# Performance work log

Hardware: AMD Instinct MI355X
Metric: run time of the kernel (lower is better)

The kernel has to match this reference:

```python
import jax, jax.numpy as jnp
import numpy as np

N, C, LM, ELEMS = 1024, 128, 16, 10   # nodes, channels, lm components (lmax=3), elements
P1, P2, P3 = 4, 12, 30                # generalized-CG path counts per correlation order
DIMS = (1, 3)                         # output irreps kept: 0e (dim 1), 1o (dim 3)


def _sparse(rng, shape, density=0.15):
    # stand-in generalized Clebsch-Gordan U tensor: fixed, sparse constants
    a = rng.standard_normal(shape).astype(np.float32)
    return jnp.asarray(a * (rng.random(shape) < density))


def setup_inputs() -> dict:
    k = jax.random.split(jax.random.key(0), 2)
    rng = np.random.default_rng(0)
    inp = {
        'x': jax.random.normal(k[0], (N, C, LM), jnp.float32),
        'species': jax.random.randint(k[1], (N,), 0, ELEMS, jnp.int32),
    }
    for i, d in enumerate(DIMS):
        inp[f'U1_{i}'] = _sparse(rng, (d, LM, P1))
        inp[f'U2_{i}'] = _sparse(rng, (d, LM, LM, P2))
        inp[f'U3_{i}'] = _sparse(rng, (d, LM, LM, LM, P3))
        for nu, p in ((1, P1), (2, P2), (3, P3)):
            inp[f'W{nu}_{i}'] = jnp.asarray((rng.standard_normal((ELEMS, p, C)) / np.sqrt(p)).astype(np.float32))
        inp[f'Wlin_{i}'] = jnp.asarray(rng.standard_normal((C, C)).astype(np.float32))
    return inp


def _sym_contract(x, species, U1, U2, U3, W1, W2, W3):
    # MACE recursive symmetric contraction, highest correlation order first.
    # x: [n, c, m] (channels factored to separate axis); species selects per-element weights.
    out = jnp.einsum('Lijmp,npc,ncm->ncLij', U3, W3[species], x)          # nu = 3 term
    out = jnp.einsum('Lijp,npc->ncLij', U2, W2[species]) + out            # add nu = 2 basis
    out = jnp.einsum('ncLij,ncj->ncLi', out, x)                           # contract one power of x
    out = jnp.einsum('Lip,npc->ncLi', U1, W1[species]) + out              # add nu = 1 basis
    return jnp.einsum('ncLi,nci->ncL', out, x)                            # [n, c, dim_L]


def _forward(x, species, U1_0, U2_0, U3_0, W1_0, W2_0, W3_0, Wlin_0,
             U1_1, U2_1, U3_1, W1_1, W2_1, W3_1, Wlin_1):
    f0 = _sym_contract(x, species, U1_0, U2_0, U3_0, W1_0, W2_0, W3_0)    # [n, C, 1]
    f1 = _sym_contract(x, species, U1_1, U2_1, U3_1, W1_1, W2_1, W3_1)    # [n, C, 3]
    s = 1.0 / float(np.sqrt(C))                                            # e3nn.Linear path norm
    y0 = jnp.einsum('nc,ck->nk', f0[..., 0], Wlin_0) * s                  # 128x0e block
    y1 = jnp.einsum('nci,ck->nki', f1, Wlin_1) * s                        # 128x1o block
    return jnp.concatenate([y0, y1.reshape(y1.shape[0], -1)], axis=-1)    # [n, 128 + 384]


def reference(x, species, U1_0, U2_0, U3_0, W1_0, W2_0, W3_0, Wlin_0,
              U1_1, U2_1, U3_1, W1_1, W2_1, W3_1, Wlin_1):
    return _forward(x, species, U1_0, U2_0, U3_0, W1_0, W2_0, W3_0, Wlin_0,
                    U1_1, U2_1, U3_1, W1_1, W2_1, W3_1, Wlin_1)
```

## Files before the change

### kernel.cpp

```cpp
#include <hip/hip_runtime.h>

typedef float v2f __attribute__((ext_vector_type(2)));

#define NN    1024
#define CC    128
#define NELEM 10
#define NQ3   816
#define NQ2   136
#define NQ    968
#define KP    48
#define QT    22

#define NL_OFF    0
#define CNT_OFF   40960
#define CALL_OFF  524288
#define F_OFF     20447232
#define UHAT_OFF  20447232

__device__ __constant__ int d_OFF2[16] = {0,16,31,45,58,70,81,91,100,108,115,121,126,130,133,135};
__device__ __constant__ int d_OFF3[16] = {0,136,256,361,452,530,596,651,696,732,760,781,796,806,812,815};

__global__ void k_usym3(const float* __restrict__ U3_0, const float* __restrict__ U3_1,
                        float* __restrict__ uhat) {
    int tid = blockIdx.x * 256 + threadIdx.x;
    if (tid >= 4 * 4096) return;
    int Lout = tid >> 12;
    int r = tid & 4095;
    int a = r >> 8, b = (r >> 4) & 15, m = r & 15;
    if (a > b || b > m) return;
    int q = d_OFF3[a] + (d_OFF2[b] - d_OFF2[a]) + (m - b);
    const float* U = (Lout == 0) ? U3_0 : U3_1;
    int L = (Lout == 0) ? 0 : (Lout - 1);
    int P[6][3] = {{a,b,m},{a,m,b},{b,a,m},{b,m,a},{m,a,b},{m,b,a}};
    float s[30];
#pragma unroll
    for (int p = 0; p < 30; ++p) s[p] = 0.f;
    for (int t = 0; t < 6; ++t) {
        bool dup = false;
        for (int u = 0; u < t; ++u)
            if (P[u][0] == P[t][0] && P[u][1] == P[t][1] && P[u][2] == P[t][2]) dup = true;
        if (dup) continue;
        const float* src = U + ((((L * 16 + P[t][0]) * 16 + P[t][1]) * 16 + P[t][2]) * 30);
#pragma unroll
        for (int p = 0; p < 30; ++p) s[p] += src[p];
    }
    float* dst = uhat + ((size_t)Lout * NQ + q) * KP;
#pragma unroll
    for (int p = 0; p < 30; ++p) dst[p] = s[p];
#pragma unroll
    for (int p = 30; p < KP; ++p) dst[p] = 0.f;
}

__global__ void k_usym2lin(const float* __restrict__ U2_0, const float* __restrict__ U2_1,
                           const float* __restrict__ U1_0, const float* __restrict__ U1_1,
                           float* __restrict__ uhat) {
    int tid = blockIdx.x * 256 + threadIdx.x;
    if (tid < 1024) {
        int Lout = tid >> 8;
        int r = tid & 255;
        int a = r >> 4, b = r & 15;
        if (a > b) return;
        int q = NQ3 + d_OFF2[a] + (b - a);
        const float* U = (Lout == 0) ? U2_0 : U2_1;
        int L = (Lout == 0) ? 0 : (Lout - 1);
        float* dst = uhat + ((size_t)Lout * NQ + q) * KP;
#pragma unroll
        for (int p = 0; p < 30; ++p) dst[p] = 0.f;
#pragma unroll
        for (int p = 0; p < 12; ++p) {
            float v = U[((L * 16 + a) * 16 + b) * 12 + p];
            if (a != b) v += U[((L * 16 + b) * 16 + a) * 12 + p];
            dst[30 + p] = v;
        }
#pragma unroll
        for (int p = 42; p < KP; ++p) dst[p] = 0.f;
    } else if (tid < 1024 + 64) {
        int s2 = tid - 1024;
        int Lout = s2 >> 4, i = s2 & 15;
        int q = NQ3 + NQ2 + i;
        const float* U = (Lout == 0) ? U1_0 : U1_1;
        int L = (Lout == 0) ? 0 : (Lout - 1);
        float* dst = uhat + ((size_t)Lout * NQ + q) * KP;
#pragma unroll
        for (int p = 0; p < 42; ++p) dst[p] = 0.f;
#pragma unroll
        for (int p = 0; p < 4; ++p) dst[42 + p] = U[(L * 16 + i) * 4 + p];
        dst[46] = 0.f; dst[47] = 0.f;
    }
}

__global__ void k_plist(const int* __restrict__ species, int* __restrict__ nodelist,
                        int* __restrict__ counts) {
    __shared__ int cnt[NELEM];
    int t = threadIdx.x;
    if (t < NELEM) cnt[t] = 0;
    __syncthreads();
    int e = species[t];
    int pos = atomicAdd(&cnt[e], 1);
    nodelist[e * NN + pos] = t;
    __syncthreads();
    if (t < NELEM) counts[t] = cnt[t];
}

__global__ __launch_bounds__(256) void k_fold(
    const float* __restrict__ uhat,
    const float* __restrict__ W1_0, const float* __restrict__ W2_0, const float* __restrict__ W3_0,
    const float* __restrict__ W1_1, const float* __restrict__ W2_1, const float* __restrict__ W3_1,
    float4* __restrict__ call4) {
    __shared__ __align__(16) float uh_lds[4][QT][KP];
    int e  = blockIdx.x / 44;
    int qt = blockIdx.x % 44;
    int t = threadIdx.x;
    {
        const float4* src4 = (const float4*)uhat;
        float4* dst4 = (float4*)uh_lds;
        for (int i = t; i < 4 * QT * 12; i += 256) {
            int l = i / (QT * 12);
            int r = i - l * (QT * 12);
            int qloc = r / 12, p4 = r % 12;
            dst4[i] = src4[((size_t)l * NQ + qt * QT + qloc) * 12 + p4];
        }
    }
    int c  = t & 127;
    int qs = t >> 7;
    float wr[2][KP];
#pragma unroll
    for (int p = 0; p < 30; ++p) {
        wr[0][p] = W3_0[(e * 30 + p) * CC + c];
        wr[1][p] = W3_1[(e * 30 + p) * CC + c];
    }
#pragma unroll
    for (int p = 0; p < 12; ++p) {
        wr[0][30 + p] = W2_0[(e * 12 + p) * CC + c];
        wr[1][30 + p] = W2_1[(e * 12 + p) * CC + c];
    }
#pragma unroll
    for (int p = 0; p < 4; ++p) {
        wr[0][42 + p] = W1_0[(e * 4 + p) * CC + c];
        wr[1][42 + p] = W1_1[(e * 4 + p) * CC + c];
    }
    wr[0][46] = wr[0][47] = wr[1][46] = wr[1][47] = 0.f;
    __syncthreads();
    size_t base = ((size_t)e * CC + c) * NQ;
    for (int j = 0; j < 11; ++j) {
        int qloc = qs * 11 + j;
        int q = qt * QT + qloc;
        float r[4];
#pragma unroll
        for (int l = 0; l < 4; ++l) {
            const float4* up = (const float4*)uh_lds[l][qloc];
            const float* w = (l == 0) ? wr[0] : wr[1];
            float acc0 = 0.f, acc1 = 0.f, acc2 = 0.f, acc3 = 0.f;
#pragma unroll
            for (int p4 = 0; p4 < 12; ++p4) {
                float4 u = up[p4];
                acc0 = fmaf(u.x, w[p4 * 4 + 0], acc0);
                acc1 = fmaf(u.y, w[p4 * 4 + 1], acc1);
                acc2 = fmaf(u.z, w[p4 * 4 + 2], acc2);
                acc3 = fmaf(u.w, w[p4 * 4 + 3], acc3);
            }
            r[l] = (acc0 + acc1) + (acc2 + acc3);
        }
        call4[base + q] = make_float4(r[0], r[1], r[2], r[3]);
    }
}

#define CUBIC(A0, A1) { \
    _Pragma("unroll") for (int a = (A0); a < (A1); ++a) { \
        _Pragma("unroll") for (int b = a; b < 16; ++b) { \
            v2f pab = xv[a] * xv[b]; \
            _Pragma("unroll") for (int m = b; m < 16; ++m) { \
                float4 w = cf_lds[q]; v2f mo = pab * xv[m]; \
                a0 += mo * w.x; a1 += mo * w.y; a2 += mo * w.z; a3 += mo * w.w; ++q; } } } }

#define QUAD(A0, A1) { \
    _Pragma("unroll") for (int a = (A0); a < (A1); ++a) { \
        _Pragma("unroll") for (int b = a; b < 16; ++b) { \
            float4 w = cf_lds[q]; v2f mo = xv[a] * xv[b]; \
            a0 += mo * w.x; a1 += mo * w.y; a2 += mo * w.z; a3 += mo * w.w; ++q; } } }

__global__ __launch_bounds__(256, 4) void k_eval(
    const float* __restrict__ x, const int* __restrict__ nodelist,
    const int* __restrict__ counts, const float4* __restrict__ call4,
    float4* __restrict__ fout) {
    __shared__ __align__(16) float4 cf_lds[NQ];
    __shared__ __align__(16) v2f part[3][64][4];
    int ec = blockIdx.x;
    int e = ec >> 7;
    int c = ec & 127;
    int cnt = counts[e];
    const float4* cf = call4 + (size_t)ec * NQ;
    int t = threadIdx.x;
    for (int i = t; i < NQ; i += 256) cf_lds[i] = cf[i];
    __syncthreads();
    int slice = t >> 6;
    int lane  = t & 63;

    for (int sb = 0; sb < cnt; sb += 128) {
        int i0 = sb + lane * 2, i1 = i0 + 1;
        bool v0i = i0 < cnt, v1i = i1 < cnt;
        int n0 = v0i ? nodelist[e * NN + i0] : 0;
        int n1 = v1i ? nodelist[e * NN + i1] : 0;
        const float4* xp0 = (const float4*)(x + ((size_t)n0 * CC + c) * 16);
        const float4* xp1 = (const float4*)(x + ((size_t)n1 * CC + c) * 16);
        float4 p0 = xp0[0], p1 = xp0[1], p2 = xp0[2], p3 = xp0[3];
        float4 q0 = xp1[0], q1 = xp1[1], q2 = xp1[2], q3 = xp1[3];
        v2f xv[16];
        xv[0]  = v2f{p0.x, q0.x}; xv[1]  = v2f{p0.y, q0.y};
        xv[2]  = v2f{p0.z, q0.z}; xv[3]  = v2f{p0.w, q0.w};
        xv[4]  = v2f{p1.x, q1.x}; xv[5]  = v2f{p1.y, q1.y};
        xv[6]  = v2f{p1.z, q1.z}; xv[7]  = v2f{p1.w, q1.w};
        xv[8]  = v2f{p2.x, q2.x}; xv[9]  = v2f{p2.y, q2.y};
        xv[10] = v2f{p2.z, q2.z}; xv[11] = v2f{p2.w, q2.w};
        xv[12] = v2f{p3.x, q3.x}; xv[13] = v2f{p3.y, q3.y};
        xv[14] = v2f{p3.z, q3.z}; xv[15] = v2f{p3.w, q3.w};
        if (!v0i) {
#pragma unroll
            for (int m = 0; m < 16; ++m) xv[m].x = 0.f;
        }
        if (!v1i) {
#pragma unroll
            for (int m = 0; m < 16; ++m) xv[m].y = 0.f;
        }
        v2f a0 = {0.f, 0.f}, a1 = {0.f, 0.f}, a2 = {0.f, 0.f}, a3 = {0.f, 0.f};
        int q;
        if (slice == 0) {
            q = 0;   CUBIC(0, 2);
        } else if (slice == 1) {
            q = 256; CUBIC(2, 4);
            q = NQ3; QUAD(0, 4);
        } else if (slice == 2) {
            q = 452; CUBIC(4, 7);
            q = NQ3 + 58; QUAD(4, 10);
        } else {
            q = 651; CUBIC(7, 16);
            q = NQ3 + 115; QUAD(10, 16);
            q = NQ3 + NQ2;
#pragma unroll
            for (int a = 0; a < 16; ++a) {
                float4 w = cf_lds[q]; v2f mo = xv[a];
                a0 += mo * w.x; a1 += mo * w.y; a2 += mo * w.z; a3 += mo * w.w; ++q;
            }
        }
        if (slice > 0) {
            part[slice - 1][lane][0] = a0; part[slice - 1][lane][1] = a1;
            part[slice - 1][lane][2] = a2; part[slice - 1][lane][3] = a3;
        }
        __syncthreads();
        if (slice == 0) {
            v2f s0 = a0 + part[0][lane][0] + part[1][lane][0] + part[2][lane][0];
            v2f s1 = a1 + part[0][lane][1] + part[1][lane][1] + part[2][lane][1];
            v2f s2 = a2 + part[0][lane][2] + part[1][lane][2] + part[2][lane][2];
            v2f s3 = a3 + part[0][lane][3] + part[1][lane][3] + part[2][lane][3];
            if (v0i) fout[(size_t)n0 * CC + c] = make_float4(s0.x, s1.x, s2.x, s3.x);
            if (v1i) fout[(size_t)n1 * CC + c] = make_float4(s0.y, s1.y, s2.y, s3.y);
        }
        __syncthreads();
    }
}

__global__ __launch_bounds__(256) void k_linear(
    const float4* __restrict__ fin, const float* __restrict__ Wlin0,
    const float* __restrict__ Wlin1, float* __restrict__ out) {
    __shared__ float4 fl[256];
    int t = threadIdx.x;
    fl[t] = fin[(size_t)blockIdx.x * 256 + t];
    __syncthreads();
    int nl = t >> 7, k = t & 127;
    int n = blockIdx.x * 2 + nl;
    float a0 = 0.f, a1 = 0.f, a2 = 0.f, a3 = 0.f;
#pragma unroll 8
    for (int c = 0; c < CC; ++c) {
        float4 f = fl[nl * CC + c];
        float w0 = Wlin0[c * CC + k];
        float w1 = Wlin1[c * CC + k];
        a0 = fmaf(f.x, w0, a0);
        a1 = fmaf(f.y, w1, a1);
        a2 = fmaf(f.z, w1, a2);
        a3 = fmaf(f.w, w1, a3);
    }
    const float s = 0.08838834764831845f;
    float* o = out + (size_t)n * 512;
    o[k] = a0 * s;
    o[128 + 3 * k + 0] = a1 * s;
    o[128 + 3 * k + 1] = a2 * s;
    o[128 + 3 * k + 2] = a3 * s;
}

extern "C" void kernel_launch(void* const* d_in, const int* in_sizes, int n_in,
                              void* d_out, int out_size, void* d_ws, size_t ws_size,
                              hipStream_t stream) {
    const float* x     = (const float*)d_in[0];
    const int*   spec  = (const int*)d_in[1];
    const float* U1_0  = (const float*)d_in[2];
    const float* U2_0  = (const float*)d_in[3];
    const float* U3_0  = (const float*)d_in[4];
    const float* W1_0  = (const float*)d_in[5];
    const float* W2_0  = (const float*)d_in[6];
    const float* W3_0  = (const float*)d_in[7];
    const float* Wl_0  = (const float*)d_in[8];
    const float* U1_1  = (const float*)d_in[9];
    const float* U2_1  = (const float*)d_in[10];
    const float* U3_1  = (const float*)d_in[11];
    const float* W1_1  = (const float*)d_in[12];
    const float* W2_1  = (const float*)d_in[13];
    const float* W3_1  = (const float*)d_in[14];
    const float* Wl_1  = (const float*)d_in[15];

    char* ws = (char*)d_ws;
    int*    nodelist = (int*)(ws + NL_OFF);
    int*    counts   = (int*)(ws + CNT_OFF);
    float4* call4    = (float4*)(ws + CALL_OFF);
    float*  uhat     = (float*)(ws + UHAT_OFF);
    float4* fbuf     = (float4*)(ws + F_OFF);

    k_usym3<<<dim3(64), dim3(256), 0, stream>>>(U3_0, U3_1, uhat);
    k_usym2lin<<<dim3(5), dim3(256), 0, stream>>>(U2_0, U2_1, U1_0, U1_1, uhat);
    k_plist<<<dim3(1), dim3(1024), 0, stream>>>(spec, nodelist, counts);
    k_fold<<<dim3(440), dim3(256), 0, stream>>>(uhat, W1_0, W2_0, W3_0,
                                                W1_1, W2_1, W3_1, call4);
    k_eval<<<dim3(1280), dim3(256), 0, stream>>>(x, nodelist, counts, call4, fbuf);
    k_linear<<<dim3(512), dim3(256), 0, stream>>>(fbuf, Wl_0, Wl_1, (float*)d_out);
}
```

Before: 88.39 us.

## Store folded coefficients in fp16, merge U kernels, retile fold, prefetch eval inputs

The per-(element,channel) folded coefficient table is now written and read as packed half2 pairs, halving its global and LDS footprint. The two U-symmetrization kernels are merged into one launch, the fold kernel uses smaller q tiles to double its block count, and the eval kernel issues its node-list and x loads before waiting on the coefficient LDS fill. The fp16 rounding of coefficients lowers accuracy and may break the tolerance. Removing the min-occupancy launch bound may also change register allocation.

```diff
diff --git a/kernel.cpp b/kernel.cpp
--- a/kernel.cpp
+++ b/kernel.cpp
@@ -1,4 +1,5 @@
 #include <hip/hip_runtime.h>
+#include <hip/hip_fp16.h>
 
 typedef float v2f __attribute__((ext_vector_type(2)));
 
@@ -9,83 +10,83 @@
 #define NQ2   136
 #define NQ    968
 #define KP    48
-#define QT    22
+#define QT    11
+#define NTILE 88
 
 #define NL_OFF    0
 #define CNT_OFF   40960
 #define CALL_OFF  524288
 #define F_OFF     20447232
-#define UHAT_OFF  20447232
+#define UHAT_OFF  10485760
 
 __device__ __constant__ int d_OFF2[16] = {0,16,31,45,58,70,81,91,100,108,115,121,126,130,133,135};
 __device__ __constant__ int d_OFF3[16] = {0,136,256,361,452,530,596,651,696,732,760,781,796,806,812,815};
 
-__global__ void k_usym3(const float* __restrict__ U3_0, const float* __restrict__ U3_1,
-                        float* __restrict__ uhat) {
-    int tid = blockIdx.x * 256 + threadIdx.x;
-    if (tid >= 4 * 4096) return;
-    int Lout = tid >> 12;
-    int r = tid & 4095;
-    int a = r >> 8, b = (r >> 4) & 15, m = r & 15;
-    if (a > b || b > m) return;
-    int q = d_OFF3[a] + (d_OFF2[b] - d_OFF2[a]) + (m - b);
-    const float* U = (Lout == 0) ? U3_0 : U3_1;
-    int L = (Lout == 0) ? 0 : (Lout - 1);
-    int P[6][3] = {{a,b,m},{a,m,b},{b,a,m},{b,m,a},{m,a,b},{m,b,a}};
-    float s[30];
-#pragma unroll
-    for (int p = 0; p < 30; ++p) s[p] = 0.f;
-    for (int t = 0; t < 6; ++t) {
-        bool dup = false;
-        for (int u = 0; u < t; ++u)
-            if (P[u][0] == P[t][0] && P[u][1] == P[t][1] && P[u][2] == P[t][2]) dup = true;
-        if (dup) continue;
-        const float* src = U + ((((L * 16 + P[t][0]) * 16 + P[t][1]) * 16 + P[t][2]) * 30);
-#pragma unroll
-        for (int p = 0; p < 30; ++p) s[p] += src[p];
-    }
-    float* dst = uhat + ((size_t)Lout * NQ + q) * KP;
-#pragma unroll
-    for (int p = 0; p < 30; ++p) dst[p] = s[p];
-#pragma unroll
-    for (int p = 30; p < KP; ++p) dst[p] = 0.f;
-}
-
-__global__ void k_usym2lin(const float* __restrict__ U2_0, const float* __restrict__ U2_1,
-                           const float* __restrict__ U1_0, const float* __restrict__ U1_1,
-                           float* __restrict__ uhat) {
-    int tid = blockIdx.x * 256 + threadIdx.x;
-    if (tid < 1024) {
-        int Lout = tid >> 8;
-        int r = tid & 255;
-        int a = r >> 4, b = r & 15;
-        if (a > b) return;
-        int q = NQ3 + d_OFF2[a] + (b - a);
-        const float* U = (Lout == 0) ? U2_0 : U2_1;
+__global__ void k_usym(const float* __restrict__ U3_0, const float* __restrict__ U3_1,
+                       const float* __restrict__ U2_0, const float* __restrict__ U2_1,
+                       const float* __restrict__ U1_0, const float* __restrict__ U1_1,
+                       float* __restrict__ uhat) {
+    if (blockIdx.x < 64) {
+        int tid = blockIdx.x * 256 + threadIdx.x;
+        int Lout = tid >> 12;
+        int r = tid & 4095;
+        int a = r >> 8, b = (r >> 4) & 15, m = r & 15;
+        if (a > b || b > m) return;
+        int q = d_OFF3[a] + (d_OFF2[b] - d_OFF2[a]) + (m - b);
+        const float* U = (Lout == 0) ? U3_0 : U3_1;
         int L = (Lout == 0) ? 0 : (Lout - 1);
+        int P[6][3] = {{a,b,m},{a,m,b},{b,a,m},{b,m,a},{m,a,b},{m,b,a}};
+        float s[30];
+#pragma unroll
+        for (int p = 0; p < 30; ++p) s[p] = 0.f;
+        for (int t = 0; t < 6; ++t) {
+            bool dup = false;
+            for (int u = 0; u < t; ++u)
+                if (P[u][0] == P[t][0] && P[u][1] == P[t][1] && P[u][2] == P[t][2]) dup = true;
+            if (dup) continue;
+            const float* src = U + ((((L * 16 + P[t][0]) * 16 + P[t][1]) * 16 + P[t][2]) * 30);
+#pragma unroll
+            for (int p = 0; p < 30; ++p) s[p] += src[p];
+        }
         float* dst = uhat + ((size_t)Lout * NQ + q) * KP;
 #pragma unroll
-        for (int p = 0; p < 30; ++p) dst[p] = 0.f;
-#pragma unroll
-        for (int p = 0; p < 12; ++p) {
-            float v = U[((L * 16 + a) * 16 + b) * 12 + p];
-            if (a != b) v += U[((L * 16 + b) * 16 + a) * 12 + p];
-            dst[30 + p] = v;
-        }
-#pragma unroll
-        for (int p = 42; p < KP; ++p) dst[p] = 0.f;
-    } else if (tid < 1024 + 64) {
-        int s2 = tid - 1024;
-        int Lout = s2 >> 4, i = s2 & 15;
-        int q = NQ3 + NQ2 + i;
-        const float* U = (Lout == 0) ? U1_0 : U1_1;
-        int L = (Lout == 0) ? 0 : (Lout - 1);
-        float* dst = uhat + ((size_t)Lout * NQ + q) * KP;
-#pragma unroll
-        for (int p = 0; p < 42; ++p) dst[p] = 0.f;
-#pragma unroll
-        for (int p = 0; p < 4; ++p) dst[42 + p] = U[(L * 16 + i) * 4 + p];
-        dst[46] = 0.f; dst[47] = 0.f;
+        for (int p = 0; p < 30; ++p) dst[p] = s[p];
+#pragma unroll
+        for (int p = 30; p < KP; ++p) dst[p] = 0.f;
+    } else {
+        int tid = (blockIdx.x - 64) * 256 + threadIdx.x;
+        if (tid < 1024) {
+            int Lout = tid >> 8;
+            int r = tid & 255;
+            int a = r >> 4, b = r & 15;
+            if (a > b) return;
+            int q = NQ3 + d_OFF2[a] + (b - a);
+            const float* U = (Lout == 0) ? U2_0 : U2_1;
+            int L = (Lout == 0) ? 0 : (Lout - 1);
+            float* dst = uhat + ((size_t)Lout * NQ + q) * KP;
+#pragma unroll
+            for (int p = 0; p < 30; ++p) dst[p] = 0.f;
+#pragma unroll
+            for (int p = 0; p < 12; ++p) {
+                float v = U[((L * 16 + a) * 16 + b) * 12 + p];
+                if (a != b) v += U[((L * 16 + b) * 16 + a) * 12 + p];
+                dst[30 + p] = v;
+            }
+#pragma unroll
+            for (int p = 42; p < KP; ++p) dst[p] = 0.f;
+        } else if (tid < 1024 + 64) {
+            int s2 = tid - 1024;
+            int Lout = s2 >> 4, i = s2 & 15;
+            int q = NQ3 + NQ2 + i;
+            const float* U = (Lout == 0) ? U1_0 : U1_1;
+            int L = (Lout == 0) ? 0 : (Lout - 1);
+            float* dst = uhat + ((size_t)Lout * NQ + q) * KP;
+#pragma unroll
+            for (int p = 0; p < 42; ++p) dst[p] = 0.f;
+#pragma unroll
+            for (int p = 0; p < 4; ++p) dst[42 + p] = U[(L * 16 + i) * 4 + p];
+            dst[46] = 0.f; dst[47] = 0.f;
+        }
     }
 }
 
@@ -106,10 +107,10 @@
     const float* __restrict__ uhat,
     const float* __restrict__ W1_0, const float* __restrict__ W2_0, const float* __restrict__ W3_0,
     const float* __restrict__ W1_1, const float* __restrict__ W2_1, const float* __restrict__ W3_1,
-    float4* __restrict__ call4) {
+    uint2* __restrict__ call4h) {
     __shared__ __align__(16) float uh_lds[4][QT][KP];
-    int e  = blockIdx.x / 44;
-    int qt = blockIdx.x % 44;
+    int e  = blockIdx.x / NTILE;
+    int qt = blockIdx.x % NTILE;
     int t = threadIdx.x;
     {
         const float4* src4 = (const float4*)uhat;
@@ -142,8 +143,9 @@
     wr[0][46] = wr[0][47] = wr[1][46] = wr[1][47] = 0.f;
     __syncthreads();
     size_t base = ((size_t)e * CC + c) * NQ;
-    for (int j = 0; j < 11; ++j) {
-        int qloc = qs * 11 + j;
+    for (int j = 0; j < 6; ++j) {
+        int qloc = qs * 6 + j;
+        if (qloc >= QT) break;
         int q = qt * QT + qloc;
         float r[4];
 #pragma unroll
@@ -161,50 +163,69 @@
             }
             r[l] = (acc0 + acc1) + (acc2 + acc3);
         }
-        call4[base + q] = make_float4(r[0], r[1], r[2], r[3]);
-    }
-}
+        __half2 h01 = __floats2half2_rn(r[0], r[1]);
+        __half2 h23 = __floats2half2_rn(r[2], r[3]);
+        uint2 v;
+        v.x = *(unsigned int*)&h01;
+        v.y = *(unsigned int*)&h23;
+        call4h[base + q] = v;
+    }
+}
+
+#define COEF(W0, W1, W2, W3) \
+    uint2 pk = cf_lds[q]; \
+    __half2 h01 = *(__half2*)&pk.x; __half2 h23 = *(__half2*)&pk.y; \
+    float W0 = __half2float(h01.x), W1 = __half2float(h01.y); \
+    float W2 = __half2float(h23.x), W3 = __half2float(h23.y);
 
 #define CUBIC(A0, A1) { \
     _Pragma("unroll") for (int a = (A0); a < (A1); ++a) { \
         _Pragma("unroll") for (int b = a; b < 16; ++b) { \
             v2f pab = xv[a] * xv[b]; \
             _Pragma("unroll") for (int m = b; m < 16; ++m) { \
-                float4 w = cf_lds[q]; v2f mo = pab * xv[m]; \
-                a0 += mo * w.x; a1 += mo * w.y; a2 += mo * w.z; a3 += mo * w.w; ++q; } } } }
+                COEF(wx, wy, wz, ww); v2f mo = pab * xv[m]; \
+                a0 += mo * wx; a1 += mo * wy; a2 += mo * wz; a3 += mo * ww; ++q; } } } }
 
 #define QUAD(A0, A1) { \
     _Pragma("unroll") for (int a = (A0); a < (A1); ++a) { \
         _Pragma("unroll") for (int b = a; b < 16; ++b) { \
-            float4 w = cf_lds[q]; v2f mo = xv[a] * xv[b]; \
-            a0 += mo * w.x; a1 += mo * w.y; a2 += mo * w.z; a3 += mo * w.w; ++q; } } }
-
-__global__ __launch_bounds__(256, 4) void k_eval(
+            COEF(wx, wy, wz, ww); v2f mo = xv[a] * xv[b]; \
+            a0 += mo * wx; a1 += mo * wy; a2 += mo * wz; a3 += mo * ww; ++q; } } }
+
+__global__ __launch_bounds__(256) void k_eval(
     const float* __restrict__ x, const int* __restrict__ nodelist,
-    const int* __restrict__ counts, const float4* __restrict__ call4,
+    const int* __restrict__ counts, const uint2* __restrict__ call4h,
     float4* __restrict__ fout) {
-    __shared__ __align__(16) float4 cf_lds[NQ];
+    __shared__ __align__(16) uint2 cf_lds[NQ];
     __shared__ __align__(16) v2f part[3][64][4];
     int ec = blockIdx.x;
     int e = ec >> 7;
     int c = ec & 127;
     int cnt = counts[e];
-    const float4* cf = call4 + (size_t)ec * NQ;
+    const float4* cf4 = (const float4*)(call4h + (size_t)ec * NQ);
     int t = threadIdx.x;
-    for (int i = t; i < NQ; i += 256) cf_lds[i] = cf[i];
-    __syncthreads();
     int slice = t >> 6;
     int lane  = t & 63;
 
+    int i0 = lane * 2, i1 = i0 + 1;
+    bool v0i = i0 < cnt, v1i = i1 < cnt;
+    int n0 = v0i ? nodelist[e * NN + i0] : 0;
+    int n1 = v1i ? nodelist[e * NN + i1] : 0;
+
+    for (int i = t; i < NQ / 2; i += 256) ((float4*)cf_lds)[i] = cf4[i];
+
     for (int sb = 0; sb < cnt; sb += 128) {
-        int i0 = sb + lane * 2, i1 = i0 + 1;
-        bool v0i = i0 < cnt, v1i = i1 < cnt;
-        int n0 = v0i ? nodelist[e * NN + i0] : 0;
-        int n1 = v1i ? nodelist[e * NN + i1] : 0;
+        if (sb > 0) {
+            i0 = sb + lane * 2; i1 = i0 + 1;
+            v0i = i0 < cnt; v1i = i1 < cnt;
+            n0 = v0i ? nodelist[e * NN + i0] : 0;
+            n1 = v1i ? nodelist[e * NN + i1] : 0;
+        }
         const float4* xp0 = (const float4*)(x + ((size_t)n0 * CC + c) * 16);
         const float4* xp1 = (const float4*)(x + ((size_t)n1 * CC + c) * 16);
         float4 p0 = xp0[0], p1 = xp0[1], p2 = xp0[2], p3 = xp0[3];
         float4 q0 = xp1[0], q1 = xp1[1], q2 = xp1[2], q3 = xp1[3];
+        if (sb == 0) __syncthreads();
         v2f xv[16];
         xv[0]  = v2f{p0.x, q0.x}; xv[1]  = v2f{p0.y, q0.y};
         xv[2]  = v2f{p0.z, q0.z}; xv[3]  = v2f{p0.w, q0.w};
@@ -238,8 +259,8 @@
             q = NQ3 + NQ2;
 #pragma unroll
             for (int a = 0; a < 16; ++a) {
-                float4 w = cf_lds[q]; v2f mo = xv[a];
-                a0 += mo * w.x; a1 += mo * w.y; a2 += mo * w.z; a3 += mo * w.w; ++q;
+                COEF(wx, wy, wz, ww); v2f mo = xv[a];
+                a0 += mo * wx; a1 += mo * wy; a2 += mo * wz; a3 += mo * ww; ++q;
             }
         }
         if (slice > 0) {
@@ -310,15 +331,14 @@
     char* ws = (char*)d_ws;
     int*    nodelist = (int*)(ws + NL_OFF);
     int*    counts   = (int*)(ws + CNT_OFF);
-    float4* call4    = (float4*)(ws + CALL_OFF);
+    uint2*  call4h   = (uint2*)(ws + CALL_OFF);
     float*  uhat     = (float*)(ws + UHAT_OFF);
     float4* fbuf     = (float4*)(ws + F_OFF);
 
-    k_usym3<<<dim3(64), dim3(256), 0, stream>>>(U3_0, U3_1, uhat);
-    k_usym2lin<<<dim3(5), dim3(256), 0, stream>>>(U2_0, U2_1, U1_0, U1_1, uhat);
+    k_usym<<<dim3(69), dim3(256), 0, stream>>>(U3_0, U3_1, U2_0, U2_1, U1_0, U1_1, uhat);
     k_plist<<<dim3(1), dim3(1024), 0, stream>>>(spec, nodelist, counts);
-    k_fold<<<dim3(440), dim3(256), 0, stream>>>(uhat, W1_0, W2_0, W3_0,
-                                                W1_1, W2_1, W3_1, call4);
-    k_eval<<<dim3(1280), dim3(256), 0, stream>>>(x, nodelist, counts, call4, fbuf);
+    k_fold<<<dim3(880), dim3(256), 0, stream>>>(uhat, W1_0, W2_0, W3_0,
+                                                W1_1, W2_1, W3_1, call4h);
+    k_eval<<<dim3(1280), dim3(256), 0, stream>>>(x, nodelist, counts, call4h, fbuf);
     k_linear<<<dim3(512), dim3(256), 0, stream>>>(fbuf, Wl_0, Wl_1, (float*)d_out);
 }
```

New measurement: 75.13 us. -15.0%, faster.
